# Kernel optimization log

Measured on AMD Instinct MI355X. Metric: run time of the kernel, lower is better.

The kernel has to match this reference:

```python
import jax, jax.numpy as jnp
import numpy as np

N_NODES = 100000
N_EDGES = 1600000
IN_FEAT = 256
HIDDEN = 128
OUT_FEAT = 64


def setup_inputs() -> dict:
    key = jax.random.key(0)
    k1, k2, k3, k4, k5, k6 = jax.random.split(key, 6)
    x = jax.random.normal(k1, (N_NODES, IN_FEAT), dtype=jnp.float32)
    edge_index = jax.random.randint(k2, (2, N_EDGES), 0, N_NODES, dtype=jnp.int64)
    # GCNConv: lin weight [in, hidden] (no bias in lin), separate bias [hidden]
    W_gc = jax.random.normal(k3, (IN_FEAT, HIDDEN), dtype=jnp.float32) / np.sqrt(IN_FEAT)
    b_gc = jnp.zeros((HIDDEN,), dtype=jnp.float32)
    # fc1: Linear(hidden, out)
    W_fc = jax.random.normal(k4, (HIDDEN, OUT_FEAT), dtype=jnp.float32) / np.sqrt(HIDDEN)
    b_fc = jax.random.normal(k5, (OUT_FEAT,), dtype=jnp.float32) * 0.01
    return {"x": x, "edge_index": edge_index, "W_gc": W_gc, "b_gc": b_gc,
            "W_fc": W_fc, "b_fc": b_fc}


def reference(x, edge_index, W_gc, b_gc, W_fc, b_fc):
    n = x.shape[0]
    # add self-loops (PyG GCNConv default)
    loop = jnp.arange(n, dtype=edge_index.dtype)
    src = jnp.concatenate([edge_index[0], loop])
    dst = jnp.concatenate([edge_index[1], loop])
    # symmetric normalization: deg over destination including self-loops
    deg = jax.ops.segment_sum(jnp.ones_like(dst, dtype=x.dtype), dst, num_segments=n)
    dinv = jnp.where(deg > 0, jax.lax.rsqrt(deg), 0.0)
    norm = dinv[src] * dinv[dst]  # [E+N]
    # transform then propagate (transform-first as in PyG GCNConv)
    h = x @ W_gc  # [N, HIDDEN]
    msg = h[src] * norm[:, None]  # [E+N, HIDDEN] -- irregular gather
    agg = jax.ops.segment_sum(msg, dst, num_segments=n) + b_gc  # scatter-add
    # fc1
    return agg @ W_fc + b_fc
```

## Files before the change

kernel.cpp:

```cpp
#include <hip/hip_runtime.h>
#include <hip/hip_bf16.h>
#include <stdint.h>

#define IN_FEAT 256
#define HIDDEN 128
#define OUT_FEAT 64
#define SCAN_B 1024

__global__ __launch_bounds__(256) void k_combine_w(
    const float* __restrict__ Wgc, const float* __restrict__ bgc,
    const float* __restrict__ Wfc, const float* __restrict__ bfc,
    float* __restrict__ Wc, float* __restrict__ bc) {
  int idx = blockIdx.x * 256 + threadIdx.x;
  if (idx < IN_FEAT * OUT_FEAT) {
    int r = idx >> 6, c = idx & 63;
    float s = 0.f;
#pragma unroll 8
    for (int j = 0; j < HIDDEN; ++j)
      s = fmaf(Wgc[r * HIDDEN + j], Wfc[j * OUT_FEAT + c], s);
    Wc[idx] = s;
  } else if (idx < IN_FEAT * OUT_FEAT + OUT_FEAT) {
    int c = idx - IN_FEAT * OUT_FEAT;
    float s = bfc[c];
    for (int j = 0; j < HIDDEN; ++j)
      s = fmaf(bgc[j], Wfc[j * OUT_FEAT + c], s);
    bc[c] = s;
  }
}

__global__ __launch_bounds__(256) void k_gemm(
    const float* __restrict__ x, const float* __restrict__ Wc,
    float* __restrict__ h2, int n) {
  __shared__ float Ws[IN_FEAT * OUT_FEAT];
  const float4* W4 = (const float4*)Wc;
  float4* Ws4 = (float4*)Ws;
  for (int i = threadIdx.x; i < IN_FEAT * OUT_FEAT / 4; i += 256) Ws4[i] = W4[i];
  __syncthreads();
  int row = blockIdx.x * 256 + threadIdx.x;
  if (row >= n) return;
  float acc[OUT_FEAT];
#pragma unroll
  for (int c = 0; c < OUT_FEAT; ++c) acc[c] = 0.f;
  const float* xr = x + (size_t)row * IN_FEAT;
  for (int k0 = 0; k0 < IN_FEAT; k0 += 4) {
    float4 xv = *(const float4*)(xr + k0);
#pragma unroll
    for (int kk = 0; kk < 4; ++kk) {
      float xs = (&xv.x)[kk];
      const float* wrow = &Ws[(k0 + kk) * OUT_FEAT];
#pragma unroll
      for (int c = 0; c < OUT_FEAT; ++c) acc[c] = fmaf(xs, wrow[c], acc[c]);
    }
  }
  float* o = h2 + (size_t)row * OUT_FEAT;
#pragma unroll
  for (int c = 0; c < OUT_FEAT; c += 4)
    *(float4*)(o + c) = make_float4(acc[c], acc[c + 1], acc[c + 2], acc[c + 3]);
}

__global__ __launch_bounds__(256) void k_count(
    const int* __restrict__ ei, int ne, int* __restrict__ cnt,
    int* __restrict__ rank) {
  int e = blockIdx.x * 256 + threadIdx.x;
  if (e < ne) {
    int dst = ei[ne + e];
    rank[e] = atomicAdd(&cnt[dst], 1);
  }
}

__global__ __launch_bounds__(SCAN_B) void k_scan1(
    const int* __restrict__ cnt, int* __restrict__ incl, int* __restrict__ bsum, int n) {
  __shared__ int sh[SCAN_B];
  int gid = blockIdx.x * SCAN_B + threadIdx.x;
  int v = (gid < n) ? cnt[gid] : 0;
  sh[threadIdx.x] = v;
  __syncthreads();
  for (int d = 1; d < SCAN_B; d <<= 1) {
    int t = (threadIdx.x >= d) ? sh[threadIdx.x - d] : 0;
    __syncthreads();
    sh[threadIdx.x] += t;
    __syncthreads();
  }
  if (gid < n) incl[gid] = sh[threadIdx.x];
  if (threadIdx.x == SCAN_B - 1) bsum[blockIdx.x] = sh[threadIdx.x];
}

__global__ __launch_bounds__(SCAN_B) void k_scan2(
    const int* __restrict__ bsum, int* __restrict__ boff, int nb) {
  __shared__ int sh[SCAN_B];
  int v = (threadIdx.x < nb) ? bsum[threadIdx.x] : 0;
  sh[threadIdx.x] = v;
  __syncthreads();
  for (int d = 1; d < SCAN_B; d <<= 1) {
    int t = (threadIdx.x >= d) ? sh[threadIdx.x - d] : 0;
    __syncthreads();
    sh[threadIdx.x] += t;
    __syncthreads();
  }
  if (threadIdx.x < nb) boff[threadIdx.x] = sh[threadIdx.x] - v;
}

__global__ __launch_bounds__(SCAN_B) void k_scan3(
    const int* __restrict__ cnt, const int* __restrict__ incl,
    const int* __restrict__ boff, int* __restrict__ rs,
    float* __restrict__ dinv, int n) {
  int gid = blockIdx.x * SCAN_B + threadIdx.x;
  if (gid < n) {
    int c = cnt[gid];
    int inc = incl[gid] + boff[gid / SCAN_B];
    rs[gid] = inc - c;
    dinv[gid] = rsqrtf((float)(c + 1));
    if (gid == n - 1) rs[n] = inc;
  }
}

__global__ __launch_bounds__(256) void k_fill(
    const int* __restrict__ ei, int ne, const int* __restrict__ rs,
    const int* __restrict__ rank, int* __restrict__ csr) {
  int e = blockIdx.x * 256 + threadIdx.x;
  if (e < ne) {
    int src = ei[e];
    int dst = ei[ne + e];
    csr[rs[dst] + rank[e]] = src;
  }
}

__global__ __launch_bounds__(256) void k_aggregate(
    const float* __restrict__ h2, const float* __restrict__ dinv,
    const float* __restrict__ bc, const int* __restrict__ rs,
    const int* __restrict__ csr, float* __restrict__ out, int n) {
  int lane = threadIdx.x & 63;
  int sub = lane >> 4;
  int fl = lane & 15;
  int wid = blockIdx.x * (blockDim.x >> 6) + (threadIdx.x >> 6);
  int nwaves = gridDim.x * (blockDim.x >> 6);
  float4 bcv = *(const float4*)(bc + fl * 4);
  for (int i = wid; i < n; i += nwaves) {
    float di = dinv[i];
    int j0 = rs[i], j1 = rs[i + 1];
    float4 acc = make_float4(0.f, 0.f, 0.f, 0.f);
#pragma unroll 2
    for (int j = j0 + sub; j < j1; j += 4) {
      int s = csr[j];
      float w = di * dinv[s];
      float4 hv = *(const float4*)(h2 + (size_t)s * OUT_FEAT + fl * 4);
      acc.x = fmaf(w, hv.x, acc.x);
      acc.y = fmaf(w, hv.y, acc.y);
      acc.z = fmaf(w, hv.z, acc.z);
      acc.w = fmaf(w, hv.w, acc.w);
    }
#pragma unroll
    for (int m = 16; m <= 32; m <<= 1) {
      acc.x += __shfl_xor(acc.x, m, 64);
      acc.y += __shfl_xor(acc.y, m, 64);
      acc.z += __shfl_xor(acc.z, m, 64);
      acc.w += __shfl_xor(acc.w, m, 64);
    }
    if (sub == 0) {
      float4 hv = *(const float4*)(h2 + (size_t)i * OUT_FEAT + fl * 4);
      float w = di * di;
      float4 r;
      r.x = fmaf(w, hv.x, acc.x + bcv.x);
      r.y = fmaf(w, hv.y, acc.y + bcv.y);
      r.z = fmaf(w, hv.z, acc.z + bcv.z);
      r.w = fmaf(w, hv.w, acc.w + bcv.w);
      *(float4*)(out + (size_t)i * OUT_FEAT + fl * 4) = r;
    }
  }
}

extern "C" void kernel_launch(void* const* d_in, const int* in_sizes, int n_in,
                              void* d_out, int out_size, void* d_ws, size_t ws_size,
                              hipStream_t stream) {
  const float* x = (const float*)d_in[0];
  const int* ei = (const int*)d_in[1];
  const float* Wgc = (const float*)d_in[2];
  const float* bgc = (const float*)d_in[3];
  const float* Wfc = (const float*)d_in[4];
  const float* bfc = (const float*)d_in[5];
  float* out = (float*)d_out;

  int N = in_sizes[0] / IN_FEAT;
  int NE = in_sizes[1] / 2;

  float* Wc = (float*)d_ws;
  float* bc = Wc + IN_FEAT * OUT_FEAT;
  float* dinv = bc + OUT_FEAT;
  int* cnt = (int*)(dinv + N);
  int* incl = cnt + N;
  int* bsum = incl + N;
  int* boff = bsum + SCAN_B;
  int* rs = boff + SCAN_B;
  int* rank = rs + ((N + 4) & ~3);
  int* csr = rank + NE;
  float* h2 = (float*)((((uintptr_t)(csr + NE)) + 15) & ~(uintptr_t)15);

  hipMemsetAsync(cnt, 0, (size_t)N * sizeof(int), stream);

  k_combine_w<<<(IN_FEAT * OUT_FEAT + OUT_FEAT + 255) / 256, 256, 0, stream>>>(
      Wgc, bgc, Wfc, bfc, Wc, bc);
  k_gemm<<<(N + 255) / 256, 256, 0, stream>>>(x, Wc, h2, N);
  k_count<<<(NE + 255) / 256, 256, 0, stream>>>(ei, NE, cnt, rank);

  int nsb = (N + SCAN_B - 1) / SCAN_B;
  k_scan1<<<nsb, SCAN_B, 0, stream>>>(cnt, incl, bsum, N);
  k_scan2<<<1, SCAN_B, 0, stream>>>(bsum, boff, nsb);
  k_scan3<<<nsb, SCAN_B, 0, stream>>>(cnt, incl, boff, rs, dinv, N);

  k_fill<<<(NE + 255) / 256, 256, 0, stream>>>(ei, NE, rs, rank, csr);
  k_aggregate<<<4096, 256, 0, stream>>>(h2, dinv, bc, rs, csr, out, N);
}
```

Before: 454.7 us.

## Rewrite dense GEMM as LDS-tiled 2D register-blocked kernel

Replaces the one-row-per-thread GEMM, which holds 64 accumulators per thread and reads x rows with poor coalescing, with a shared-memory tiled GEMM. Each block stages a 128-row by 32-K tile of x (transposed) and a 32x64 tile of W in LDS. Each thread then computes an 8x4 output tile. This is meant to improve global-load coalescing, cut register pressure and raise occupancy, at the cost of more block-level synchronisation and possible LDS bank conflicts on the transposed stores.

```diff
diff --git a/kernel.cpp b/kernel.cpp
--- a/kernel.cpp
+++ b/kernel.cpp
@@ -6,6 +6,9 @@
 #define HIDDEN 128
 #define OUT_FEAT 64
 #define SCAN_B 1024
+
+#define BROWS 128
+#define BK 32
 
 __global__ __launch_bounds__(256) void k_combine_w(
     const float* __restrict__ Wgc, const float* __restrict__ bgc,
@@ -31,31 +34,71 @@
 __global__ __launch_bounds__(256) void k_gemm(
     const float* __restrict__ x, const float* __restrict__ Wc,
     float* __restrict__ h2, int n) {
-  __shared__ float Ws[IN_FEAT * OUT_FEAT];
-  const float4* W4 = (const float4*)Wc;
-  float4* Ws4 = (float4*)Ws;
-  for (int i = threadIdx.x; i < IN_FEAT * OUT_FEAT / 4; i += 256) Ws4[i] = W4[i];
-  __syncthreads();
-  int row = blockIdx.x * 256 + threadIdx.x;
-  if (row >= n) return;
-  float acc[OUT_FEAT];
-#pragma unroll
-  for (int c = 0; c < OUT_FEAT; ++c) acc[c] = 0.f;
-  const float* xr = x + (size_t)row * IN_FEAT;
-  for (int k0 = 0; k0 < IN_FEAT; k0 += 4) {
-    float4 xv = *(const float4*)(xr + k0);
-#pragma unroll
-    for (int kk = 0; kk < 4; ++kk) {
-      float xs = (&xv.x)[kk];
-      const float* wrow = &Ws[(k0 + kk) * OUT_FEAT];
-#pragma unroll
-      for (int c = 0; c < OUT_FEAT; ++c) acc[c] = fmaf(xs, wrow[c], acc[c]);
-    }
-  }
-  float* o = h2 + (size_t)row * OUT_FEAT;
-#pragma unroll
-  for (int c = 0; c < OUT_FEAT; c += 4)
-    *(float4*)(o + c) = make_float4(acc[c], acc[c + 1], acc[c + 2], acc[c + 3]);
+  __shared__ float A_lds[BK][BROWS];
+  __shared__ float W_lds[BK][OUT_FEAT];
+
+  int tid = threadIdx.x;
+  int ty = tid >> 4;
+  int tx = tid & 15;
+  int row0 = blockIdx.x * BROWS;
+
+  int srow = tid >> 1;
+  int shalf = tid & 1;
+  int wk = tid >> 4;
+
+  float acc[8][4];
+#pragma unroll
+  for (int i = 0; i < 8; ++i)
+#pragma unroll
+    for (int j = 0; j < 4; ++j) acc[i][j] = 0.f;
+
+  for (int k0 = 0; k0 < IN_FEAT; k0 += BK) {
+    float4 av[4];
+    int grow = row0 + srow;
+    if (grow < n) {
+      const float4* src = (const float4*)(x + (size_t)grow * IN_FEAT + k0 + shalf * 16);
+#pragma unroll
+      for (int p = 0; p < 4; ++p) av[p] = src[p];
+    } else {
+#pragma unroll
+      for (int p = 0; p < 4; ++p) av[p] = make_float4(0.f, 0.f, 0.f, 0.f);
+    }
+    float4 wv0 = *(const float4*)(Wc + (size_t)(k0 + (tid >> 4)) * OUT_FEAT + (tid & 15) * 4);
+    float4 wv1 = *(const float4*)(Wc + (size_t)(k0 + 16 + (tid >> 4)) * OUT_FEAT + (tid & 15) * 4);
+    __syncthreads();
+#pragma unroll
+    for (int p = 0; p < 4; ++p) {
+      int kk = shalf * 16 + p * 4;
+      A_lds[kk + 0][srow] = av[p].x;
+      A_lds[kk + 1][srow] = av[p].y;
+      A_lds[kk + 2][srow] = av[p].z;
+      A_lds[kk + 3][srow] = av[p].w;
+    }
+    *(float4*)(&W_lds[tid >> 4][(tid & 15) * 4]) = wv0;
+    *(float4*)(&W_lds[16 + (tid >> 4)][(tid & 15) * 4]) = wv1;
+    __syncthreads();
+
+#pragma unroll 4
+    for (int k = 0; k < BK; ++k) {
+      float4 a0 = *(const float4*)(&A_lds[k][ty * 8]);
+      float4 a1 = *(const float4*)(&A_lds[k][ty * 8 + 4]);
+      float4 w = *(const float4*)(&W_lds[k][tx * 4]);
+      float ar[8] = {a0.x, a0.y, a0.z, a0.w, a1.x, a1.y, a1.z, a1.w};
+      float wr[4] = {w.x, w.y, w.z, w.w};
+#pragma unroll
+      for (int i = 0; i < 8; ++i)
+#pragma unroll
+        for (int j = 0; j < 4; ++j) acc[i][j] = fmaf(ar[i], wr[j], acc[i][j]);
+    }
+  }
+
+#pragma unroll
+  for (int i = 0; i < 8; ++i) {
+    int row = row0 + ty * 8 + i;
+    if (row < n)
+      *(float4*)(h2 + (size_t)row * OUT_FEAT + tx * 4) =
+          make_float4(acc[i][0], acc[i][1], acc[i][2], acc[i][3]);
+  }
 }
 
 __global__ __launch_bounds__(256) void k_count(
@@ -199,7 +242,7 @@
 
   k_combine_w<<<(IN_FEAT * OUT_FEAT + OUT_FEAT + 255) / 256, 256, 0, stream>>>(
       Wgc, bgc, Wfc, bfc, Wc, bc);
-  k_gemm<<<(N + 255) / 256, 256, 0, stream>>>(x, Wc, h2, N);
+  k_gemm<<<(N + BROWS - 1) / BROWS, 256, 0, stream>>>(x, Wc, h2, N);
   k_count<<<(NE + 255) / 256, 256, 0, stream>>>(ei, NE, cnt, rank);
 
   int nsb = (N + SCAN_B - 1) / SCAN_B;
```

Result: faster. 396.8 us (-12.7%).
